# Kernel optimization log

Hardware: AMD Instinct MI355X
Metric: run time of the kernel (lower is better)

## Reference

```python
import jax, jax.numpy as jnp
import numpy as np

D_MODEL = 1024
N_HEADS = 16
D_K = D_MODEL // N_HEADS
SEQ = 2048
BATCH = 4
THETA = 10000.0


def setup_inputs() -> dict:
    key = jax.random.key(0)
    k_x, k_q, k_k, k_v, k_o = jax.random.split(key, 5)
    std = (2.0 / (D_MODEL + D_MODEL)) ** 0.5
    def trunc(k):
        # truncated normal on [-3*std, 3*std]
        return std * jax.random.truncated_normal(k, -3.0, 3.0, (D_MODEL, D_MODEL), jnp.float32)
    return {
        "x": jax.random.normal(k_x, (BATCH, SEQ, D_MODEL), jnp.float32),
        "token_positions": jnp.arange(SEQ, dtype=jnp.int32),
        "Wq": trunc(k_q),
        "Wk": trunc(k_k),
        "Wv": trunc(k_v),
        "Wo": trunc(k_o),
    }


def _rope(x, cos, sin):
    # x: [b, h, s, d_k]; cos/sin: [s, d_k/2] broadcast over b,h
    x_even = x[..., ::2]
    x_odd = x[..., 1::2]
    out_even = x_even * cos - x_odd * sin
    out_odd = x_even * sin + x_odd * cos
    # interleave back: stack -> [..., d_k/2, 2] -> [..., d_k]
    return jnp.stack([out_even, out_odd], axis=-1).reshape(x.shape)


def reference(x, token_positions, Wq, Wk, Wv, Wo):
    B, S, D = x.shape
    H, dk = N_HEADS, D_K

    def proj(W):
        y = jnp.einsum("bsi,oi->bso", x, W)
        return y.reshape(B, S, H, dk).transpose(0, 2, 1, 3)  # b h s d

    q, k, v = proj(Wq), proj(Wk), proj(Wv)

    # RoPE caches
    freq = 1.0 / THETA ** (jnp.arange(0, dk, 2, dtype=jnp.float32) / dk)  # [dk/2]
    pos = token_positions.astype(jnp.float32)  # [S]
    freqs = pos[:, None] * freq[None, :]  # [S, dk/2]
    cos, sin = jnp.cos(freqs), jnp.sin(freqs)
    q = _rope(q, cos, sin)
    k = _rope(k, cos, sin)

    scale = 1.0 / jnp.sqrt(jnp.float32(dk))
    scores = jnp.einsum("bhqd,bhkd->bhqk", q, k) * scale  # [b,h,S,S]
    causal = jnp.tril(jnp.ones((S, S), dtype=bool))
    scores = jnp.where(causal, scores, -jnp.inf)
    # naive stable softmax (max-subtract / exp / sum), matching source
    s_max = jnp.max(scores, axis=-1, keepdims=True)
    e = jnp.exp(scores - s_max)
    attn = e / jnp.sum(e, axis=-1, keepdims=True)
    out = jnp.einsum("bhqk,bhkd->bhqd", attn, v)  # [b,h,S,dk]
    out = out.transpose(0, 2, 1, 3).reshape(B, S, D)
    return jnp.einsum("bsi,oi->bso", out, Wo)
```

## Files before the change

kernel.cpp:

```cpp
#include <hip/hip_runtime.h>

#define SEQ   2048
#define BATCH 4
#define NH    16
#define DM    1024
#define MTOT  (BATCH*SEQ)

typedef unsigned short u16;
typedef unsigned int   u32;
typedef __attribute__((ext_vector_type(8)))  __bf16 bf16x8;
typedef __attribute__((ext_vector_type(4)))  float  f32x4;
typedef __attribute__((ext_vector_type(16))) float  f32x16;
typedef __attribute__((address_space(1))) u32 as1_u32;
typedef __attribute__((address_space(3))) u32 as3_u32;

__device__ __forceinline__ u16 f2bf(float f) {
  union { float f; u32 u; } c; c.f = f;
  return (u16)((c.u + 0x7fffu + ((c.u >> 16) & 1u)) >> 16);
}

__global__ void cast_bf16_k(const float* __restrict__ in, u16* __restrict__ out, int n4) {
  int i = blockIdx.x * blockDim.x + threadIdx.x;
  if (i < n4) {
    float4 v = reinterpret_cast<const float4*>(in)[i];
    ushort4 o;
    o.x = f2bf(v.x); o.y = f2bf(v.y); o.z = f2bf(v.z); o.w = f2bf(v.w);
    reinterpret_cast<ushort4*>(out)[i] = o;
  }
}

__global__ void rope_tab_k(const int* __restrict__ pos, float2* __restrict__ tab) {
  int i = blockIdx.x * blockDim.x + threadIdx.x;
  if (i < SEQ * 32) {
    int s = i >> 5, j = i & 31;
    float p = (float)pos[s];
    float fr = powf(10000.f, -(float)j / 32.f);
    float a = p * fr;
    tab[i] = make_float2(cosf(a), sinf(a));
  }
}

template<int EPI>
__global__ __launch_bounds__(256)
void gemm_bt(const u16* __restrict__ A,
             const u16* __restrict__ B0, const u16* __restrict__ B1, const u16* __restrict__ B2,
             float* __restrict__ outF,
             u16* __restrict__ Qh, u16* __restrict__ Kh, u16* __restrict__ Vt,
             const float2* __restrict__ tab) {
  const int K = DM, N = DM;
  __shared__ u16 lsA[128 * 32];
  __shared__ u16 lsB[128 * 32];
  const int t = threadIdx.x;
  const int lane = t & 63;
  const int wid = t >> 6;
  const int wr = wid >> 1, wc = wid & 1;
  const int m0 = blockIdx.y * 128, n0 = blockIdx.x * 128;
  const int z = blockIdx.z;
  const u16* Bt = (z == 0) ? B0 : (z == 1 ? B1 : B2);

  f32x4 acc[4][4] = {};

  const int srow = t >> 2;
  const int scol = (t & 3) * 8;
  const u16* gA = A + (size_t)(m0 + srow) * K + scol;
  const u16* gB = Bt + (size_t)(n0 + srow) * K + scol;
  const u32 lo = (u32)t * 16u;

  for (int kt = 0; kt < K; kt += 32) {
    __builtin_amdgcn_global_load_lds((const as1_u32*)(gA + kt),
                                     (as3_u32*)((char*)lsA + lo), 16, 0, 0);
    __builtin_amdgcn_global_load_lds((const as1_u32*)(gA + (size_t)64 * K + kt),
                                     (as3_u32*)((char*)lsA + 4096 + lo), 16, 0, 0);
    __builtin_amdgcn_global_load_lds((const as1_u32*)(gB + kt),
                                     (as3_u32*)((char*)lsB + lo), 16, 0, 0);
    __builtin_amdgcn_global_load_lds((const as1_u32*)(gB + (size_t)64 * K + kt),
                                     (as3_u32*)((char*)lsB + 4096 + lo), 16, 0, 0);
    __syncthreads();
    bf16x8 af[4], bfr[4];
#pragma unroll
    for (int mt = 0; mt < 4; ++mt)
      af[mt] = *(const bf16x8*)&lsA[(wr * 64 + mt * 16 + (lane & 15)) * 32 + (lane >> 4) * 8];
#pragma unroll
    for (int nt = 0; nt < 4; ++nt)
      bfr[nt] = *(const bf16x8*)&lsB[(wc * 64 + nt * 16 + (lane & 15)) * 32 + (lane >> 4) * 8];
#pragma unroll
    for (int mt = 0; mt < 4; ++mt)
#pragma unroll
      for (int nt = 0; nt < 4; ++nt)
        acc[mt][nt] = __builtin_amdgcn_mfma_f32_16x16x32_bf16(af[mt], bfr[nt], acc[mt][nt], 0, 0, 0);
    __syncthreads();
  }

#pragma unroll
  for (int mt = 0; mt < 4; ++mt) {
    const int gmb = m0 + wr * 64 + mt * 16 + (lane >> 4) * 4;
#pragma unroll
    for (int nt = 0; nt < 4; ++nt) {
      const int gn = n0 + wc * 64 + nt * 16 + (lane & 15);
#pragma unroll
      for (int r = 0; r < 4; ++r) {
        float v = acc[mt][nt][r];
        if (EPI == 0) {
          outF[(size_t)(gmb + r) * N + gn] = v;
        } else {
          const int row = gmb + r;
          const int b = row >> 11, s = row & (SEQ - 1);
          const int h = gn >> 6, dd = gn & 63;
          if (z < 2) {
            float p = __shfl_xor(v, 1);
            const float2 cs = tab[(s << 5) + (dd >> 1)];
            float o = ((lane & 1) == 0) ? (v * cs.x - p * cs.y) : (p * cs.y + v * cs.x);
            if (z == 0) o *= 0.18033688011112042f;
            u16* dst = z ? Kh : Qh;
            dst[((size_t)((b * NH + h) * SEQ + s) << 6) + dd] = f2bf(o);
          } else {
            Vt[((size_t)((b * NH + h) << 6) + dd) * SEQ + s] = f2bf(v);
          }
        }
      }
    }
  }
}

__global__ __launch_bounds__(256)
void attn_k(const u16* __restrict__ Qh, const u16* __restrict__ Kh,
            const u16* __restrict__ Vt, u16* __restrict__ AO) {
  __shared__ u16 lsK[2][64 * 64];
  __shared__ u16 lsV[2][64 * 64];
  const int t = threadIdx.x, lane = t & 63, w = t >> 6;
  const int hiL = lane >> 5;
  const int q31 = lane & 31;
  const int bid = blockIdx.x;
  const int bh = bid & 63, b = bh >> 4, h = bh & 15;
  const int chunk_blk = 15 - (bid >> 6);
  const int qb_blk = chunk_blk * 128;
  const int tendB = (qb_blk + 127) >> 6;
  const int qbase = qb_blk + w * 32;
  const int tendW = (qbase + 31) >> 6;
  const u16* Qp = Qh + (size_t)bh * SEQ * 64;
  const u16* Kp = Kh + (size_t)bh * SEQ * 64;
  const u16* Vp = Vt + (size_t)bh * 64 * SEQ;

  bf16x8 qa[4];
#pragma unroll
  for (int kc = 0; kc < 4; ++kc)
    qa[kc] = *(const bf16x8*)(Qp + (size_t)(qbase + q31) * 64 + kc * 16 + hiL * 8);

  f32x16 O0 = {}, O1 = {};
  float m = -1e30f, l = 0.f;

#define STAGE(bf, kt_)                                                                  \
  {                                                                                     \
    const int k0s = (kt_) * 64;                                                         \
    _Pragma("unroll")                                                                   \
    for (int hh = 0; hh < 2; ++hh) {                                                    \
      const int idx = hh * 256 + t;                                                     \
      const int row = idx >> 3;                                                         \
      const int cb = ((idx & 7) << 4) ^ ((row & 7) << 4);                               \
      __builtin_amdgcn_global_load_lds((const as1_u32*)(Kp + (size_t)(k0s + row) * 64 + (cb >> 1)), \
                                       (as3_u32*)((char*)&lsK[bf][0] + idx * 16), 16, 0, 0); \
      __builtin_amdgcn_global_load_lds((const as1_u32*)(Vp + (size_t)row * SEQ + k0s + (cb >> 1)), \
                                       (as3_u32*)((char*)&lsV[bf][0] + idx * 16), 16, 0, 0); \
    }                                                                                   \
  }

  STAGE(0, 0);
  __syncthreads();
  int cur = 0;

  for (int kt = 0; kt <= tendB; ++kt) {
    if (kt < tendB) STAGE(cur ^ 1, kt + 1);

    if (kt <= tendW) {
      const int k0 = kt * 64;
      const int swz = (q31 & 7) << 4;

      f32x16 S0 = {}, S1 = {};
#pragma unroll
      for (int kc = 0; kc < 4; ++kc) {
        const int cb = (kc * 32 + hiL * 16) ^ swz;
        bf16x8 ka = *(const bf16x8*)&lsK[cur][q31 * 64 + (cb >> 1)];
        S0 = __builtin_amdgcn_mfma_f32_32x32x16_bf16(ka, qa[kc], S0, 0, 0, 0);
      }
#pragma unroll
      for (int kc = 0; kc < 4; ++kc) {
        const int cb = (kc * 32 + hiL * 16) ^ swz;
        bf16x8 ka = *(const bf16x8*)&lsK[cur][(32 + q31) * 64 + (cb >> 1)];
        S1 = __builtin_amdgcn_mfma_f32_32x32x16_bf16(ka, qa[kc], S1, 0, 0, 0);
      }

      if (kt == tendW) {
        const int qg = qbase + q31;
#pragma unroll
        for (int r = 0; r < 16; ++r) {
          const int kg = k0 + (r & 3) + 8 * (r >> 2) + 4 * hiL;
          S0[r] = (kg > qg) ? -1e30f : S0[r];
          S1[r] = (kg + 32 > qg) ? -1e30f : S1[r];
        }
      }

      float vmax = -1e30f;
#pragma unroll
      for (int r = 0; r < 16; ++r) {
        vmax = fmaxf(vmax, S0[r]);
        vmax = fmaxf(vmax, S1[r]);
      }
      vmax = fmaxf(vmax, __shfl_xor(vmax, 32));

      if (vmax > m + 7.f) {
        const float al = exp2f(m - vmax);
        m = vmax; l *= al;
#pragma unroll
        for (int r = 0; r < 16; ++r) { O0[r] *= al; O1[r] *= al; }
      }

      float rs = 0.f;
#pragma unroll
      for (int r = 0; r < 16; ++r) {
        const float p0 = exp2f(S0[r] - m);
        const float p1 = exp2f(S1[r] - m);
        S0[r] = p0; S1[r] = p1;
        rs += p0 + p1;
      }
      l += rs;

      bf16x8 pb[4];
#define PACKKC(SV, kb, OUT)                                                         \
      {                                                                             \
        u32 qL0, qL1, qH0, qH1;                                                     \
        asm("v_cvt_pk_bf16_f32 %0, %1, %2" : "=v"(qL0) : "v"(SV[8*(kb)+0]), "v"(SV[8*(kb)+1])); \
        asm("v_cvt_pk_bf16_f32 %0, %1, %2" : "=v"(qL1) : "v"(SV[8*(kb)+2]), "v"(SV[8*(kb)+3])); \
        asm("v_cvt_pk_bf16_f32 %0, %1, %2" : "=v"(qH0) : "v"(SV[8*(kb)+4]), "v"(SV[8*(kb)+5])); \
        asm("v_cvt_pk_bf16_f32 %0, %1, %2" : "=v"(qH1) : "v"(SV[8*(kb)+6]), "v"(SV[8*(kb)+7])); \
        const u32 sA = hiL ? qL0 : qH0;                                             \
        const u32 sB = hiL ? qL1 : qH1;                                             \
        const u32 rA = (u32)__shfl_xor((int)sA, 32);                                \
        const u32 rB = (u32)__shfl_xor((int)sB, 32);                                \
        union { u32 wds[4]; bf16x8 v; } uu;                                         \
        uu.wds[0] = hiL ? rA : qL0;                                                 \
        uu.wds[1] = hiL ? rB : qL1;                                                 \
        uu.wds[2] = hiL ? qH0 : rA;                                                 \
        uu.wds[3] = hiL ? qH1 : rB;                                                 \
        OUT = uu.v;                                                                 \
      }
      PACKKC(S0, 0, pb[0])
      PACKKC(S0, 1, pb[1])
      PACKKC(S1, 0, pb[2])
      PACKKC(S1, 1, pb[3])
#undef PACKKC

#pragma unroll
      for (int kc = 0; kc < 4; ++kc) {
        const int cb = (kc * 32 + hiL * 16) ^ swz;
        bf16x8 va0 = *(const bf16x8*)&lsV[cur][q31 * 64 + (cb >> 1)];
        bf16x8 va1 = *(const bf16x8*)&lsV[cur][(32 + q31) * 64 + (cb >> 1)];
        O0 = __builtin_amdgcn_mfma_f32_32x32x16_bf16(va0, pb[kc], O0, 0, 0, 0);
        O1 = __builtin_amdgcn_mfma_f32_32x32x16_bf16(va1, pb[kc], O1, 0, 0, 0);
      }
    }

    __syncthreads();
    cur ^= 1;
  }

  l += __shfl_xor(l, 32);
  const float inv = 1.f / l;
  const int s = qbase + q31;
  u16* dst = AO + ((size_t)(b * SEQ + s) * NH + h) * 64;
#pragma unroll
  for (int rp = 0; rp < 8; ++rp) {
    const int r = rp * 2;
    const int d = (r & 3) + 8 * (r >> 2) + 4 * hiL;
    u32 w0, w1;
    asm("v_cvt_pk_bf16_f32 %0, %1, %2" : "=v"(w0) : "v"(O0[r] * inv), "v"(O0[r + 1] * inv));
    asm("v_cvt_pk_bf16_f32 %0, %1, %2" : "=v"(w1) : "v"(O1[r] * inv), "v"(O1[r + 1] * inv));
    *reinterpret_cast<u32*>(dst + d) = w0;
    *reinterpret_cast<u32*>(dst + 32 + d) = w1;
  }
}

extern "C" void kernel_launch(void* const* d_in, const int* in_sizes, int n_in,
                              void* d_out, int out_size, void* d_ws, size_t ws_size,
                              hipStream_t stream) {
  const float* x  = (const float*)d_in[0];
  const int*   pos = (const int*)d_in[1];
  const float* Wq = (const float*)d_in[2];
  const float* Wk = (const float*)d_in[3];
  const float* Wv = (const float*)d_in[4];
  const float* Wo = (const float*)d_in[5];
  float* out = (float*)d_out;
  char* ws = (char*)d_ws;
  const size_t MB = 1024 * 1024;
  if (ws_size < 73 * MB) return;

  u16* xb  = (u16*)(ws);
  u16* wqb = (u16*)(ws + 16 * MB);
  u16* wkb = (u16*)(ws + 18 * MB);
  u16* wvb = (u16*)(ws + 20 * MB);
  u16* wob = (u16*)(ws + 22 * MB);
  u16* Qh  = (u16*)(ws + 24 * MB);
  u16* Kh  = (u16*)(ws + 40 * MB);
  u16* Vt  = (u16*)(ws + 56 * MB);
  float2* tab = (float2*)(ws + 72 * MB);
  u16* AO = xb;

  cast_bf16_k<<<(MTOT * DM / 4) / 256, 256, 0, stream>>>(x, xb, MTOT * DM / 4);
  cast_bf16_k<<<(DM * DM / 4) / 256, 256, 0, stream>>>(Wq, wqb, DM * DM / 4);
  cast_bf16_k<<<(DM * DM / 4) / 256, 256, 0, stream>>>(Wk, wkb, DM * DM / 4);
  cast_bf16_k<<<(DM * DM / 4) / 256, 256, 0, stream>>>(Wv, wvb, DM * DM / 4);
  cast_bf16_k<<<(DM * DM / 4) / 256, 256, 0, stream>>>(Wo, wob, DM * DM / 4);
  rope_tab_k<<<(SEQ * 32) / 256, 256, 0, stream>>>(pos, tab);

  gemm_bt<1><<<dim3(8, 64, 3), 256, 0, stream>>>(xb, wqb, wkb, wvb, nullptr, Qh, Kh, Vt, tab);
  attn_k<<<dim3(1024), 256, 0, stream>>>(Qh, Kh, Vt, AO);
  gemm_bt<0><<<dim3(8, 64, 1), 256, 0, stream>>>(AO, wob, wob, wob, out, nullptr, nullptr, nullptr, nullptr);
}
```

Baseline: 230.2 us.

## Replace GEMM with 256x256 tile, 8-wave, double-buffered swizzled LDS pipeline

Swaps the 128x128 single-buffered GEMM for a 256x256-tile kernel with 512 threads. It uses 128KB of LDS holding double-buffered 64-wide K slices, XOR-swizzled to avoid bank conflicts. Loads for the next K step are interleaved between quarter-tile MFMA phases, using explicit vmcnt/lgkmcnt waits, barriers and s_setprio, so copies overlap compute. The goal is to hide global load latency and raise operand reuse. In exchange it runs one block per CU, and with only 384 and 128 blocks the grids may leave some CUs idle, especially for the output projection.

```diff
diff --git a/kernel.cpp b/kernel.cpp
--- a/kernel.cpp
+++ b/kernel.cpp
@@ -41,71 +41,130 @@
 }
 
 template<int EPI>
-__global__ __launch_bounds__(256)
-void gemm_bt(const u16* __restrict__ A,
-             const u16* __restrict__ B0, const u16* __restrict__ B1, const u16* __restrict__ B2,
-             float* __restrict__ outF,
-             u16* __restrict__ Qh, u16* __restrict__ Kh, u16* __restrict__ Vt,
-             const float2* __restrict__ tab) {
-  const int K = DM, N = DM;
-  __shared__ u16 lsA[128 * 32];
-  __shared__ u16 lsB[128 * 32];
-  const int t = threadIdx.x;
-  const int lane = t & 63;
-  const int wid = t >> 6;
-  const int wr = wid >> 1, wc = wid & 1;
-  const int m0 = blockIdx.y * 128, n0 = blockIdx.x * 128;
-  const int z = blockIdx.z;
-  const u16* Bt = (z == 0) ? B0 : (z == 1 ? B1 : B2);
-
-  f32x4 acc[4][4] = {};
-
-  const int srow = t >> 2;
-  const int scol = (t & 3) * 8;
-  const u16* gA = A + (size_t)(m0 + srow) * K + scol;
-  const u16* gB = Bt + (size_t)(n0 + srow) * K + scol;
-  const u32 lo = (u32)t * 16u;
-
-  for (int kt = 0; kt < K; kt += 32) {
-    __builtin_amdgcn_global_load_lds((const as1_u32*)(gA + kt),
-                                     (as3_u32*)((char*)lsA + lo), 16, 0, 0);
-    __builtin_amdgcn_global_load_lds((const as1_u32*)(gA + (size_t)64 * K + kt),
-                                     (as3_u32*)((char*)lsA + 4096 + lo), 16, 0, 0);
-    __builtin_amdgcn_global_load_lds((const as1_u32*)(gB + kt),
-                                     (as3_u32*)((char*)lsB + lo), 16, 0, 0);
-    __builtin_amdgcn_global_load_lds((const as1_u32*)(gB + (size_t)64 * K + kt),
-                                     (as3_u32*)((char*)lsB + 4096 + lo), 16, 0, 0);
-    __syncthreads();
-    bf16x8 af[4], bfr[4];
-#pragma unroll
-    for (int mt = 0; mt < 4; ++mt)
-      af[mt] = *(const bf16x8*)&lsA[(wr * 64 + mt * 16 + (lane & 15)) * 32 + (lane >> 4) * 8];
-#pragma unroll
-    for (int nt = 0; nt < 4; ++nt)
-      bfr[nt] = *(const bf16x8*)&lsB[(wc * 64 + nt * 16 + (lane & 15)) * 32 + (lane >> 4) * 8];
-#pragma unroll
-    for (int mt = 0; mt < 4; ++mt)
-#pragma unroll
-      for (int nt = 0; nt < 4; ++nt)
-        acc[mt][nt] = __builtin_amdgcn_mfma_f32_16x16x32_bf16(af[mt], bfr[nt], acc[mt][nt], 0, 0, 0);
-    __syncthreads();
-  }
-
-#pragma unroll
-  for (int mt = 0; mt < 4; ++mt) {
-    const int gmb = m0 + wr * 64 + mt * 16 + (lane >> 4) * 4;
-#pragma unroll
-    for (int nt = 0; nt < 4; ++nt) {
-      const int gn = n0 + wc * 64 + nt * 16 + (lane & 15);
+__global__ __launch_bounds__(512, 1)
+void gemm8(const u16* __restrict__ A,
+           const u16* __restrict__ B0, const u16* __restrict__ B1, const u16* __restrict__ B2,
+           float* __restrict__ outF,
+           u16* __restrict__ Qh, u16* __restrict__ Kh, u16* __restrict__ Vt,
+           const float2* __restrict__ tab) {
+  const int K = DM;
+  const int NT = K / 64;
+  __shared__ u16 ls[65536];
+  char* lsb = (char*)ls;
+  const int t = threadIdx.x, lane = t & 63, wid = t >> 6;
+  const int wr = wid >> 2, wc = wid & 3;
+  const int n0 = blockIdx.x * 256, m0 = blockIdx.y * 256;
+  const int z = (EPI == 1) ? (n0 >> 10) : 0;
+  const int nb = (EPI == 1) ? (n0 & 1023) : n0;
+  const u16* Bt = (EPI == 1) ? ((z == 0) ? B0 : (z == 1 ? B1 : B2)) : B0;
+
+  f32x4 acc[8][4] = {};
+
+#define STAGEH(buf, hsel, kt)                                                       \
+  {                                                                                 \
+    _Pragma("unroll")                                                               \
+    for (int hh = 0; hh < 2; ++hh) {                                                \
+      const int idx = hh * 512 + t;                                                 \
+      const int row = idx >> 3, slot = idx & 7;                                     \
+      const int sg = slot ^ (row & 7);                                              \
+      const u16* src = ((hsel) < 2)                                                 \
+        ? A  + (size_t)(m0 + (hsel) * 128 + row) * K + (kt) * 64 + sg * 8           \
+        : Bt + (size_t)(nb + ((hsel) - 2) * 128 + row) * K + (kt) * 64 + sg * 8;    \
+      char* dst = lsb + (((hsel) < 2) ? 0 : 65536) + (buf) * 32768 +                \
+                  (((hsel) & 1) * 16384) + idx * 16;                                \
+      __builtin_amdgcn_global_load_lds((const as1_u32*)src, (as3_u32*)dst, 16, 0, 0); \
+    }                                                                               \
+  }
+
+  bf16x8 af[4][2];
+  bf16x8 bfr[2][2][2];
+  const int lslot = lane >> 4;
+  const int lswz = lane & 7;
+#define READ_A(buf, mh)                                                             \
+  _Pragma("unroll")                                                                 \
+  for (int mt = 0; mt < 4; ++mt)                                                    \
+    _Pragma("unroll")                                                               \
+    for (int kk = 0; kk < 2; ++kk) {                                                \
+      const int r = (mh) * 64 + mt * 16 + (lane & 15);                              \
+      af[mt][kk] = *(const bf16x8*)(lsb + (buf) * 32768 + wr * 16384 + r * 128 +    \
+                                    ((((kk << 2) + lslot) ^ lswz) << 4));           \
+    }
+#define READ_B(buf, nh)                                                             \
+  _Pragma("unroll")                                                                 \
+  for (int nt = 0; nt < 2; ++nt)                                                    \
+    _Pragma("unroll")                                                               \
+    for (int kk = 0; kk < 2; ++kk) {                                                \
+      const int r = (wc & 1) * 64 + (nh) * 32 + nt * 16 + (lane & 15);              \
+      bfr[nh][nt][kk] = *(const bf16x8*)(lsb + 65536 + (buf) * 32768 +              \
+                                         (wc >> 1) * 16384 + r * 128 +              \
+                                         ((((kk << 2) + lslot) ^ lswz) << 4));      \
+    }
+#define MFMA_Q(mh, nh)                                                              \
+  __builtin_amdgcn_s_setprio(1);                                                    \
+  _Pragma("unroll")                                                                 \
+  for (int mt = 0; mt < 4; ++mt)                                                    \
+    _Pragma("unroll")                                                               \
+    for (int nt = 0; nt < 2; ++nt)                                                  \
+      _Pragma("unroll")                                                             \
+      for (int kk = 0; kk < 2; ++kk)                                                \
+        acc[(mh) * 4 + mt][(nh) * 2 + nt] = __builtin_amdgcn_mfma_f32_16x16x32_bf16(\
+            af[mt][kk], bfr[nh][nt][kk], acc[(mh) * 4 + mt][(nh) * 2 + nt], 0, 0, 0);\
+  __builtin_amdgcn_s_setprio(0);
+#define LGKM0 asm volatile("s_waitcnt lgkmcnt(0)" ::: "memory");                    \
+              __builtin_amdgcn_sched_barrier(0);
+#define BAR   __builtin_amdgcn_s_barrier();
+
+  STAGEH(0, 0, 0) STAGEH(0, 1, 0) STAGEH(0, 2, 0) STAGEH(0, 3, 0)
+  STAGEH(1, 0, 1)
+
+  for (int kt = 0; kt < NT; ++kt) {
+    const int c = kt & 1;
+    if (kt + 1 < NT) STAGEH(c ^ 1, 1, kt + 1)
+    asm volatile("s_waitcnt vmcnt(4)" ::: "memory");
+    __builtin_amdgcn_sched_barrier(0);
+    BAR
+    __builtin_amdgcn_sched_barrier(0);
+    READ_A(c, 0)
+    READ_B(c, 0)
+    LGKM0
+    MFMA_Q(0, 0)
+    BAR
+    READ_B(c, 1)
+    if (kt + 1 < NT) STAGEH(c ^ 1, 2, kt + 1)
+    LGKM0
+    MFMA_Q(0, 1)
+    BAR
+    READ_A(c, 1)
+    if (kt + 1 < NT) STAGEH(c ^ 1, 3, kt + 1)
+    LGKM0
+    MFMA_Q(1, 0)
+    BAR
+    if (kt + 2 < NT) STAGEH(c, 0, kt + 2)
+    MFMA_Q(1, 1)
+  }
+#undef STAGEH
+#undef READ_A
+#undef READ_B
+#undef MFMA_Q
+#undef LGKM0
+#undef BAR
+
+#pragma unroll
+  for (int mi = 0; mi < 8; ++mi) {
+    const int gmb = m0 + wr * 128 + mi * 16 + (lane >> 4) * 4;
+#pragma unroll
+    for (int ni = 0; ni < 4; ++ni) {
+      const int gn = n0 + wc * 64 + ni * 16 + (lane & 15);
 #pragma unroll
       for (int r = 0; r < 4; ++r) {
-        float v = acc[mt][nt][r];
+        float v = acc[mi][ni][r];
         if (EPI == 0) {
-          outF[(size_t)(gmb + r) * N + gn] = v;
+          outF[(size_t)(gmb + r) * DM + gn] = v;
         } else {
           const int row = gmb + r;
           const int b = row >> 11, s = row & (SEQ - 1);
-          const int h = gn >> 6, dd = gn & 63;
+          const int gnl = gn & 1023;
+          const int h = gnl >> 6, dd = gnl & 63;
           if (z < 2) {
             float p = __shfl_xor(v, 1);
             const float2 cs = tab[(s << 5) + (dd >> 1)];
@@ -311,7 +370,7 @@
   cast_bf16_k<<<(DM * DM / 4) / 256, 256, 0, stream>>>(Wo, wob, DM * DM / 4);
   rope_tab_k<<<(SEQ * 32) / 256, 256, 0, stream>>>(pos, tab);
 
-  gemm_bt<1><<<dim3(8, 64, 3), 256, 0, stream>>>(xb, wqb, wkb, wvb, nullptr, Qh, Kh, Vt, tab);
+  gemm8<1><<<dim3(12, 32), 512, 0, stream>>>(xb, wqb, wkb, wvb, nullptr, Qh, Kh, Vt, tab);
   attn_k<<<dim3(1024), 256, 0, stream>>>(Qh, Kh, Vt, AO);
-  gemm_bt<0><<<dim3(8, 64, 1), 256, 0, stream>>>(AO, wob, wob, wob, out, nullptr, nullptr, nullptr, nullptr);
-}
+  gemm8<0><<<dim3(4, 32), 512, 0, stream>>>(AO, wob, wob, wob, out, nullptr, nullptr, nullptr, nullptr);
+}
```

Result: slower. 241.2 us (+4.8%).

## Fuse prep kernels into one launch and deepen attention K/V prefetch to two stages

Applied to the files above, without the earlier changes.

Merges the five bf16 cast kernels and the RoPE table kernel into a single prep launch, removing several kernel launches and their tail gaps. In the attention kernel, both LDS buffers are preloaded before the loop, and each iteration waits with a vmcnt count so one stage can stay in flight. The next-next tile is issued after the end-of-iteration barrier. This aims to hide global-to-LDS latency better, but relies on precise vmcnt counting, and an off-by-one would cause races.

```diff
diff --git a/kernel.cpp b/kernel.cpp
--- a/kernel.cpp
+++ b/kernel.cpp
@@ -19,25 +19,39 @@
   return (u16)((c.u + 0x7fffu + ((c.u >> 16) & 1u)) >> 16);
 }
 
-__global__ void cast_bf16_k(const float* __restrict__ in, u16* __restrict__ out, int n4) {
-  int i = blockIdx.x * blockDim.x + threadIdx.x;
-  if (i < n4) {
-    float4 v = reinterpret_cast<const float4*>(in)[i];
-    ushort4 o;
-    o.x = f2bf(v.x); o.y = f2bf(v.y); o.z = f2bf(v.z); o.w = f2bf(v.w);
-    reinterpret_cast<ushort4*>(out)[i] = o;
-  }
-}
-
-__global__ void rope_tab_k(const int* __restrict__ pos, float2* __restrict__ tab) {
-  int i = blockIdx.x * blockDim.x + threadIdx.x;
-  if (i < SEQ * 32) {
-    int s = i >> 5, j = i & 31;
-    float p = (float)pos[s];
-    float fr = powf(10000.f, -(float)j / 32.f);
-    float a = p * fr;
-    tab[i] = make_float2(cosf(a), sinf(a));
-  }
+__global__ __launch_bounds__(256)
+void prep_k(const float* __restrict__ x,  const float* __restrict__ Wq,
+            const float* __restrict__ Wk, const float* __restrict__ Wv,
+            const float* __restrict__ Wo, const int* __restrict__ pos,
+            u16* __restrict__ xb,  u16* __restrict__ wqb, u16* __restrict__ wkb,
+            u16* __restrict__ wvb, u16* __restrict__ wob, float2* __restrict__ tab) {
+  const int NX4 = MTOT * DM / 4;
+  const int NW4 = DM * DM / 4;
+  const int i = blockIdx.x * blockDim.x + threadIdx.x;
+  int j = i;
+  const float* src = nullptr; u16* dst = nullptr;
+  if (j < NX4) { src = x; dst = xb; }
+  else {
+    j -= NX4;
+    if (j < NW4) { src = Wq; dst = wqb; }
+    else if (j < 2 * NW4) { src = Wk; dst = wkb; j -= NW4; }
+    else if (j < 3 * NW4) { src = Wv; dst = wvb; j -= 2 * NW4; }
+    else if (j < 4 * NW4) { src = Wo; dst = wob; j -= 3 * NW4; }
+    else {
+      j -= 4 * NW4;
+      if (j < SEQ * 32) {
+        const int s = j >> 5, jj = j & 31;
+        const float p = (float)pos[s];
+        const float fr = powf(10000.f, -(float)jj / 32.f);
+        tab[j] = make_float2(cosf(p * fr), sinf(p * fr));
+      }
+      return;
+    }
+  }
+  float4 v = reinterpret_cast<const float4*>(src)[j];
+  ushort4 o;
+  o.x = f2bf(v.x); o.y = f2bf(v.y); o.z = f2bf(v.z); o.w = f2bf(v.w);
+  reinterpret_cast<ushort4*>(dst)[j] = o;
 }
 
 template<int EPI>
@@ -164,12 +178,14 @@
     }                                                                                   \
   }
 
-  STAGE(0, 0);
-  __syncthreads();
-  int cur = 0;
+  STAGE(0, 0)
+  STAGE(1, 1)
 
   for (int kt = 0; kt <= tendB; ++kt) {
-    if (kt < tendB) STAGE(cur ^ 1, kt + 1);
+    const int cur = kt & 1;
+    asm volatile("s_waitcnt vmcnt(4)" ::: "memory");
+    __builtin_amdgcn_sched_barrier(0);
+    __builtin_amdgcn_s_barrier();
 
     if (kt <= tendW) {
       const int k0 = kt * 64;
@@ -259,8 +275,8 @@
       }
     }
 
-    __syncthreads();
-    cur ^= 1;
+    __builtin_amdgcn_s_barrier();
+    if (kt + 2 <= tendB) STAGE(cur, kt + 2)
   }
 
   l += __shfl_xor(l, 32);
@@ -304,13 +320,9 @@
   float2* tab = (float2*)(ws + 72 * MB);
   u16* AO = xb;
 
-  cast_bf16_k<<<(MTOT * DM / 4) / 256, 256, 0, stream>>>(x, xb, MTOT * DM / 4);
-  cast_bf16_k<<<(DM * DM / 4) / 256, 256, 0, stream>>>(Wq, wqb, DM * DM / 4);
-  cast_bf16_k<<<(DM * DM / 4) / 256, 256, 0, stream>>>(Wk, wkb, DM * DM / 4);
-  cast_bf16_k<<<(DM * DM / 4) / 256, 256, 0, stream>>>(Wv, wvb, DM * DM / 4);
-  cast_bf16_k<<<(DM * DM / 4) / 256, 256, 0, stream>>>(Wo, wob, DM * DM / 4);
-  rope_tab_k<<<(SEQ * 32) / 256, 256, 0, stream>>>(pos, tab);
-
+  const int NPREP = MTOT * DM / 4 + 4 * (DM * DM / 4) + SEQ * 32;
+  prep_k<<<(NPREP + 255) / 256, 256, 0, stream>>>(x, Wq, Wk, Wv, Wo, pos,
+                                                  xb, wqb, wkb, wvb, wob, tab);
   gemm_bt<1><<<dim3(8, 64, 3), 256, 0, stream>>>(xb, wqb, wkb, wvb, nullptr, Qh, Kh, Vt, tab);
   attn_k<<<dim3(1024), 256, 0, stream>>>(Qh, Kh, Vt, AO);
   gemm_bt<0><<<dim3(8, 64, 1), 256, 0, stream>>>(AO, wob, wob, wob, out, nullptr, nullptr, nullptr, nullptr);
```

Result: faster. 222.4 us (-3.4%).
